# Kernel optimization log

Hardware: AMD Instinct MI355X
Metric: run time of the kernel (lower is better)

## Reference

```python
import jax, jax.numpy as jnp
import numpy as np

MAX_S, MIN_S, MAX_R = 3.0, 0.5, 3.0
A = (MAX_S - MIN_S) / 2.0   # 1.25
B = (MAX_S + MIN_S) / 2.0   # 1.75
C = (MAX_R - 1.0) / 2.0     # 1.0
D = (MAX_R + 1.0) / 2.0     # 2.0

# 3x3 kernel base points, row-major: dim0 = dy, dim1 = dx, shape [2, 9]
BASE = jnp.array([[-1, -1], [-1, 0], [-1, 1], [0, -1], [0, 0], [0, 1],
                  [1, -1], [1, 0], [1, 1]], dtype=jnp.float32).T


def conv2d(x, w, b=None):
    y = jax.lax.conv_general_dilated(x, w, window_strides=(1, 1),
                                     padding=((1, 1), (1, 1)),
                                     dimension_numbers=('NCHW', 'OIHW', 'NCHW'))
    if b is not None:
        y = y + b[None, :, None, None]
    return y


def setup_inputs() -> dict:
    key = jax.random.key(0)
    ks = jax.random.split(key, 8)
    return {
        'x': jax.random.normal(ks[0], (8, 64, 128, 128), jnp.float32),
        'w_main': jax.random.normal(ks[1], (64, 64, 3, 3), jnp.float32) * 0.05,
        'w_rot': jax.random.normal(ks[2], (2, 64, 3, 3), jnp.float32) * 0.05,
        'b_rot': jax.random.normal(ks[3], (2,), jnp.float32) * 0.05,
        'w_str': jax.random.normal(ks[4], (1, 64, 3, 3), jnp.float32) * 0.05,
        'b_str': jax.random.normal(ks[5], (1,), jnp.float32) * 0.05,
        'w_whl': jax.random.normal(ks[6], (1, 64, 3, 3), jnp.float32) * 0.05,
        'b_whl': jax.random.normal(ks[7], (1,), jnp.float32) * 0.05,
    }


def reference(x, w_main, w_rot, b_rot, w_str, b_str, w_whl, b_whl):
    b, c, H, W = x.shape
    K = 9
    # --- offset generation ---
    rot = conv2d(x, w_rot, b_rot)                     # [b,2,H,W]
    sin, cos = rot[:, 0], rot[:, 1]
    norm = jnp.sqrt(sin ** 2 + cos ** 2 + 1e-6)
    sin, cos = sin / norm, cos / norm
    r = jnp.tanh(conv2d(x, w_str, b_str))[:, 0] * A + B   # [b,H,W]
    wr = jnp.tanh(conv2d(x, w_whl, b_whl))[:, 0] * C + D  # [b,H,W]
    ky, kx = BASE[0], BASE[1]                             # [9]
    kyb = ky[None, :, None, None]
    kxb = kx[None, :, None, None]
    o0 = kyb * (wr * r)[:, None]                          # [b,9,H,W]
    o1 = kxb * wr[:, None]
    sinb, cosb = sin[:, None], cos[:, None]
    dy = cosb * o0 + sinb * o1 - kyb                      # rotation then subtract base
    dx = -sinb * o0 + cosb * o1 - kxb
    # --- deformable sampling positions (stride=1, pad=1, dil=1) ---
    py = jnp.arange(H, dtype=x.dtype)[None, None, :, None] + kyb + dy  # [b,9,H,W]
    px = jnp.arange(W, dtype=x.dtype)[None, None, None, :] + kxb + dx
    y0f = jnp.floor(py); x0f = jnp.floor(px)
    ly = py - y0f; lx = px - x0f
    y0 = y0f.astype(jnp.int32); x0 = x0f.astype(jnp.int32)
    x_flat = x.reshape(b, c, H * W)

    def gather(yi, xi, wgt):
        valid = (yi >= 0) & (yi < H) & (xi >= 0) & (xi < W)
        idx = jnp.clip(yi, 0, H - 1) * W + jnp.clip(xi, 0, W - 1)
        g = jnp.take_along_axis(x_flat, idx.reshape(b, 1, -1), axis=2)
        g = g.reshape(b, c, K, H, W)
        return g * (wgt * valid)[:, None]

    val = (gather(y0, x0, (1 - ly) * (1 - lx))
           + gather(y0, x0 + 1, (1 - ly) * lx)
           + gather(y0 + 1, x0, ly * (1 - lx))
           + gather(y0 + 1, x0 + 1, ly * lx))          # [b,c,9,H,W]
    # final 3x3 conv over sampled points == contraction over (c, k)
    out = jnp.einsum('bckhw,ock->bohw', val, w_main.reshape(w_main.shape[0], c, K))
    return out
```

## Files before the change

kernel.cpp:

```cpp
#include <hip/hip_runtime.h>
#include <hip/hip_bf16.h>
#include <hip/hip_fp16.h>
#include <math.h>

#define HH 128
#define WW 128
#define HWSZ (HH*WW)
#define CH 64
#define OC 64
#define NB 8
#define RG 28
#define RPX (RG*RG)

#define XT_BYTES   (16777216u)
#define OFFS_BYTES (2097152u)

typedef _Float16 f16x8 __attribute__((ext_vector_type(8)));
typedef __attribute__((ext_vector_type(4))) float f32x4_t;

__global__ __launch_bounds__(256) void transpose_kernel(
    const float* __restrict__ x, const float* __restrict__ w_main,
    __half* __restrict__ xT, __half* __restrict__ wmT2)
{
    const int t = threadIdx.x;
    const int i = blockIdx.x;
    if (i >= 2048) {
        const int base = (i - 2048) * 4096 + t * 16;
        #pragma unroll
        for (int j = 0; j < 16; ++j) {
            const int e = base + j;
            const int k = e >> 12;
            const int r = e & 4095;
            const int o = r >> 6;
            const int c = r & 63;
            wmT2[e] = __float2half(w_main[(size_t)o * (CH * 9) + c * 9 + k]);
        }
        return;
    }
    __shared__ float tile[64][65];
    const int b = i & 7;
    const int j = i >> 3;
    const int h  = j >> 1;
    const int w0 = (j & 1) * 64;
    const float* xb = x + (size_t)b * CH * HWSZ + h * WW + w0;
    {
        const int w = t & 63, c0 = (t >> 6) * 16;
        #pragma unroll
        for (int jj = 0; jj < 16; ++jj)
            tile[c0 + jj][w] = xb[(size_t)(c0 + jj) * HWSZ + w];
    }
    __syncthreads();
    {
        const int c = t & 63, wq = t >> 6;
        __half* o = xT + ((size_t)b * HWSZ + h * WW + w0) * 64;
        #pragma unroll
        for (int jj = 0; jj < 16; ++jj) {
            const int w = wq * 16 + jj;
            o[(size_t)w * 64 + c] = __float2half(tile[c][w]);
        }
    }
}

__global__ __launch_bounds__(256) void offsets_kernel(
    const float* __restrict__ x,
    const float* __restrict__ w_rot,
    const float* __restrict__ w_str,
    const float* __restrict__ w_whl,
    float4* __restrict__ part)
{
    __shared__ float xs[8][4][WW];
    const int t  = threadIdx.x;
    const int i  = blockIdx.x;
    const int b  = i & 7;
    const int rp = (i >> 3) & 63;
    const int cg = i >> 9;
    const int h0 = rp * 2;
    const int c0 = cg * 8;
    const float* xb = x + (size_t)b * CH * HWSZ;
    #pragma unroll
    for (int jj = 0; jj < 4; ++jj) {
        const int u   = t + jj * 256;
        const int ch  = u >> 7;
        const int rem = u & 127;
        const int row = rem >> 5;
        const int w4  = (rem & 31) * 4;
        const int grow = h0 - 1 + row;
        float4 v = make_float4(0.f, 0.f, 0.f, 0.f);
        if (grow >= 0 && grow < HH)
            v = *(const float4*)&xb[((size_t)(c0 + ch) * HH + grow) * WW + w4];
        *(float4*)&xs[ch][row][w4] = v;
    }
    __syncthreads();
    const int r = t >> 7, w = t & 127;
    const int wl = max(w - 1, 0), wr2 = min(w + 1, WW - 1);
    const float ml = (w > 0) ? 1.f : 0.f, mr = (w < WW - 1) ? 1.f : 0.f;
    float a0 = 0.f, a1 = 0.f, a2 = 0.f, a3 = 0.f;
    #pragma unroll
    for (int ch = 0; ch < 8; ++ch) {
        const int cc = c0 + ch;
        #pragma unroll
        for (int dy = 0; dy < 3; ++dy) {
            const float* row_ = &xs[ch][r + dy][0];
            const float nl = row_[wl] * ml;
            const float nc = row_[w];
            const float nr = row_[wr2] * mr;
            const int d0 = cc * 9 + dy * 3;
            a0 = fmaf(nl, w_rot[d0 + 0], a0); a0 = fmaf(nc, w_rot[d0 + 1], a0); a0 = fmaf(nr, w_rot[d0 + 2], a0);
            a1 = fmaf(nl, w_rot[576 + d0 + 0], a1); a1 = fmaf(nc, w_rot[576 + d0 + 1], a1); a1 = fmaf(nr, w_rot[576 + d0 + 2], a1);
            a2 = fmaf(nl, w_str[d0 + 0], a2); a2 = fmaf(nc, w_str[d0 + 1], a2); a2 = fmaf(nr, w_str[d0 + 2], a2);
            a3 = fmaf(nl, w_whl[d0 + 0], a3); a3 = fmaf(nc, w_whl[d0 + 1], a3); a3 = fmaf(nr, w_whl[d0 + 2], a3);
        }
    }
    part[((size_t)cg * NB + b) * HWSZ + (h0 + r) * WW + w] = make_float4(a0, a1, a2, a3);
}

__global__ __launch_bounds__(256) void reduce_kernel(
    const float4* __restrict__ part,
    const float* __restrict__ b_rot, const float* __restrict__ b_str,
    const float* __restrict__ b_whl, float4* __restrict__ offs)
{
    const int i = blockIdx.x * 256 + threadIdx.x;
    float4 s = make_float4(0.f, 0.f, 0.f, 0.f);
    #pragma unroll
    for (int cg = 0; cg < 8; ++cg) {
        const float4 p = part[(size_t)cg * NB * HWSZ + i];
        s.x += p.x; s.y += p.y; s.z += p.z; s.w += p.w;
    }
    float sv = s.x + b_rot[0], cv = s.y + b_rot[1];
    const float inv = 1.0f / sqrtf(sv * sv + cv * cv + 1e-6f);
    const float rr = tanhf(s.z + b_str[0]) * 1.25f + 1.75f;
    const float wq = tanhf(s.w + b_whl[0]) * 1.0f + 2.0f;
    offs[i] = make_float4(sv * inv, cv * inv, wq * rr, wq);
}

__global__ __launch_bounds__(256, 3) void deform_kernel(
    const __half* __restrict__ xT, const __half* __restrict__ wmT2,
    const float4* __restrict__ offs, float* __restrict__ out)
{
    __shared__ union {
        uint4 xs[RPX * 4];
        float ots[64][67];
    } sh;
    const int t  = threadIdx.x;
    const int wv = t >> 6;
    const int l  = t & 63;
    const int lm = l & 15;
    const int lg = l >> 4;
    const int i  = blockIdx.x;
    const int b  = i & 7;
    const int tile = i >> 3;
    const int w0 = (tile & 15) * 8;
    const int h0 = (tile >> 4) * 8;
    const int pi = wv * 16 + lm;
    const int h = h0 + (pi >> 3);
    const int w = w0 + (pi & 7);
    const float4 o4 = offs[(size_t)b * HWSZ + h * WW + w];
    const float sv = o4.x, cv = o4.y, av = o4.z, wvl = o4.w;
    const float hh  = (float)h;
    const float wwf = (float)w;
    const __half* xb = xT + (size_t)b * HWSZ * 64;

    int ti[9], td[9];
    __half2 w2[9][4];
    #pragma unroll
    for (int k = 0; k < 9; ++k) {
        const float kyf = (float)(k / 3) - 1.f;
        const float kxf = (float)(k % 3) - 1.f;
        const float o0v = kyf * av;
        const float o1v = kxf * wvl;
        const float pyf = hh  + cv * o0v + sv * o1v;
        const float pxf = wwf - sv * o0v + cv * o1v;
        const float y0f = floorf(pyf), x0f = floorf(pxf);
        const float ly = pyf - y0f, lx = pxf - x0f;
        const int y0 = (int)y0f, x0i = (int)x0f;
        const int y1 = y0 + 1, x1 = x0i + 1;
        const bool vy0 = (y0 >= 0) && (y0 < HH);
        const bool vy1 = (y1 >= 0) && (y1 < HH);
        const bool vx0 = (x0i >= 0) && (x0i < WW);
        const bool vx1 = (x1 >= 0) && (x1 < WW);
        w2[k][0] = __float2half2_rn((1.f - ly) * (1.f - lx) * ((vy0 && vx0) ? 1.f : 0.f));
        w2[k][1] = __float2half2_rn((1.f - ly) * lx         * ((vy0 && vx1) ? 1.f : 0.f));
        w2[k][2] = __float2half2_rn(ly * (1.f - lx)         * ((vy1 && vx0) ? 1.f : 0.f));
        w2[k][3] = __float2half2_rn(ly * lx                 * ((vy1 && vx1) ? 1.f : 0.f));
        const int iy0 = min(max(y0, 0), HH - 1), iy1 = min(max(y1, 0), HH - 1);
        const int ix0 = min(max(x0i, 0), WW - 1), ix1 = min(max(x1, 0), WW - 1);
        ti[k] = (iy0 - (h0 - 10)) * RG + (ix0 - (w0 - 10));
        td[k] = (ix1 - ix0) | ((iy1 - iy0) << 1);
    }

    f32x4_t acc0 = {0.f, 0.f, 0.f, 0.f};
    f32x4_t acc1 = acc0, acc2 = acc0, acc3 = acc0;

    for (int g = 0; g < 2; ++g) {
        __syncthreads();
        for (int u = t; u < RPX * 4; u += 256) {
            const int pxu = u >> 2, q = u & 3;
            const int lr = pxu / RG;
            const int lc = pxu - lr * RG;
            const int gy = min(max(h0 - 10 + lr, 0), HH - 1);
            const int gx = min(max(w0 - 10 + lc, 0), WW - 1);
            sh.xs[pxu * 4 + (q ^ (pxu & 3))] =
                *(const uint4*)(xb + (size_t)(gy * WW + gx) * 64 + g * 32 + q * 8);
        }
        __syncthreads();
        const int cb0 = g * 32 + lg * 8;
        #pragma unroll
        for (int k = 0; k < 9; ++k) {
            const int i00 = ti[k];
            const int dxx = td[k] & 1;
            const int dyy = (td[k] >> 1) * RG;
            const int i01 = i00 + dxx;
            const int i10 = i00 + dyy;
            const int i11 = i10 + dxx;
            union Q { uint4 q; __half2 h2[4]; };
            Q q00, q01, q10, q11;
            q00.q = sh.xs[i00 * 4 + (lg ^ (i00 & 3))];
            q01.q = sh.xs[i01 * 4 + (lg ^ (i01 & 3))];
            q10.q = sh.xs[i10 * 4 + (lg ^ (i10 & 3))];
            q11.q = sh.xs[i11 * 4 + (lg ^ (i11 & 3))];
            union { __half2 h2[4]; f16x8 v; } af;
            #pragma unroll
            for (int j = 0; j < 4; ++j) {
                af.h2[j] = __hfma2(q00.h2[j], w2[k][0],
                           __hfma2(q01.h2[j], w2[k][1],
                           __hfma2(q10.h2[j], w2[k][2],
                           __hmul2(q11.h2[j], w2[k][3]))));
            }
            const __half* wp = wmT2 + ((size_t)k * 64 + lm) * 64 + cb0;
            const f16x8 bf0 = *(const f16x8*)(wp);
            const f16x8 bf1 = *(const f16x8*)(wp + 1024);
            const f16x8 bf2v = *(const f16x8*)(wp + 2048);
            const f16x8 bf3 = *(const f16x8*)(wp + 3072);
            acc0 = __builtin_amdgcn_mfma_f32_16x16x32_f16(af.v, bf0,  acc0, 0, 0, 0);
            acc1 = __builtin_amdgcn_mfma_f32_16x16x32_f16(af.v, bf1,  acc1, 0, 0, 0);
            acc2 = __builtin_amdgcn_mfma_f32_16x16x32_f16(af.v, bf2v, acc2, 0, 0, 0);
            acc3 = __builtin_amdgcn_mfma_f32_16x16x32_f16(af.v, bf3,  acc3, 0, 0, 0);
        }
    }
    __syncthreads();
    const int pxw = wv * 16 + lg * 4;
    #pragma unroll
    for (int rg2 = 0; rg2 < 4; ++rg2) {
        sh.ots[pxw + rg2][ 0 + lm] = acc0[rg2];
        sh.ots[pxw + rg2][16 + lm] = acc1[rg2];
        sh.ots[pxw + rg2][32 + lm] = acc2[rg2];
        sh.ots[pxw + rg2][48 + lm] = acc3[rg2];
    }
    __syncthreads();
    const int oo = t >> 2;
    const int q  = (t & 3) * 16;
    #pragma unroll
    for (int j2 = 0; j2 < 4; ++j2) {
        const int px = q + j2 * 4;
        float4 v = make_float4(sh.ots[px + 0][oo], sh.ots[px + 1][oo],
                               sh.ots[px + 2][oo], sh.ots[px + 3][oo]);
        *(float4*)&out[((size_t)b * OC + oo) * HWSZ +
                       (h0 + (px >> 3)) * WW + w0 + (px & 7)] = v;
    }
}

extern "C" void kernel_launch(void* const* d_in, const int* in_sizes, int n_in,
                              void* d_out, int out_size, void* d_ws, size_t ws_size,
                              hipStream_t stream)
{
    const float* x      = (const float*)d_in[0];
    const float* w_main = (const float*)d_in[1];
    const float* w_rot  = (const float*)d_in[2];
    const float* b_rot  = (const float*)d_in[3];
    const float* w_str  = (const float*)d_in[4];
    const float* b_str  = (const float*)d_in[5];
    const float* w_whl  = (const float*)d_in[6];
    const float* b_whl  = (const float*)d_in[7];
    float* out = (float*)d_out;

    char* ws = (char*)d_ws;
    __half*  xT   = (__half*)ws;
    float4*  offs = (float4*)(ws + XT_BYTES);
    __half*  wmT2 = (__half*)(ws + XT_BYTES + OFFS_BYTES);
    float4*  part = (float4*)d_out;

    transpose_kernel<<<dim3(2057), 256, 0, stream>>>(x, w_main, xT, wmT2);
    offsets_kernel<<<dim3(4096), 256, 0, stream>>>(x, w_rot, w_str, w_whl, part);
    reduce_kernel<<<dim3(NB * HWSZ / 256), 256, 0, stream>>>(
        part, b_rot, b_str, b_whl, offs);
    deform_kernel<<<dim3(2048), 256, 0, stream>>>(xT, wmT2, offs, out);
}
```

Measured before the change: 213.1 us.

## Fuse transpose, offset conv and reduction into one pre-kernel; change LDS swizzle

Merges the transpose, offset-convolution and partial-sum reduction kernels into a single launch. Each offset block now loops over all 8 channel groups itself, so the partial-sum buffer and the separate reduce pass go away. This removes two launches and the partials round trip through global memory, but leaves only 512 offset blocks, each doing eight times more serial work. The deform kernel's LDS XOR swizzle now keys on (index>>1)&3 to change its bank-conflict pattern.

```diff
diff --git a/kernel.cpp b/kernel.cpp
--- a/kernel.cpp
+++ b/kernel.cpp
@@ -18,14 +18,21 @@
 typedef _Float16 f16x8 __attribute__((ext_vector_type(8)));
 typedef __attribute__((ext_vector_type(4))) float f32x4_t;
 
-__global__ __launch_bounds__(256) void transpose_kernel(
+__global__ __launch_bounds__(256) void pre_kernel(
     const float* __restrict__ x, const float* __restrict__ w_main,
-    __half* __restrict__ xT, __half* __restrict__ wmT2)
+    const float* __restrict__ w_rot, const float* __restrict__ w_str,
+    const float* __restrict__ w_whl,
+    const float* __restrict__ b_rot, const float* __restrict__ b_str,
+    const float* __restrict__ b_whl,
+    __half* __restrict__ xT, __half* __restrict__ wmT2,
+    float4* __restrict__ offs)
 {
+    __shared__ float shmem[64 * 65];
     const int t = threadIdx.x;
     const int i = blockIdx.x;
-    if (i >= 2048) {
-        const int base = (i - 2048) * 4096 + t * 16;
+
+    if (i >= 2560) {
+        const int base = (i - 2560) * 4096 + t * 16;
         #pragma unroll
         for (int j = 0; j < 16; ++j) {
             const int e = base + j;
@@ -37,100 +44,84 @@
         }
         return;
     }
-    __shared__ float tile[64][65];
-    const int b = i & 7;
-    const int j = i >> 3;
-    const int h  = j >> 1;
-    const int w0 = (j & 1) * 64;
-    const float* xb = x + (size_t)b * CH * HWSZ + h * WW + w0;
-    {
-        const int w = t & 63, c0 = (t >> 6) * 16;
-        #pragma unroll
-        for (int jj = 0; jj < 16; ++jj)
-            tile[c0 + jj][w] = xb[(size_t)(c0 + jj) * HWSZ + w];
-    }
-    __syncthreads();
-    {
-        const int c = t & 63, wq = t >> 6;
-        __half* o = xT + ((size_t)b * HWSZ + h * WW + w0) * 64;
-        #pragma unroll
-        for (int jj = 0; jj < 16; ++jj) {
-            const int w = wq * 16 + jj;
-            o[(size_t)w * 64 + c] = __float2half(tile[c][w]);
-        }
-    }
-}
-
-__global__ __launch_bounds__(256) void offsets_kernel(
-    const float* __restrict__ x,
-    const float* __restrict__ w_rot,
-    const float* __restrict__ w_str,
-    const float* __restrict__ w_whl,
-    float4* __restrict__ part)
-{
-    __shared__ float xs[8][4][WW];
-    const int t  = threadIdx.x;
-    const int i  = blockIdx.x;
+
+    if (i >= 512) {
+        float (*tile)[65] = (float(*)[65])shmem;
+        const int it = i - 512;
+        const int b = it & 7;
+        const int j = it >> 3;
+        const int h  = j >> 1;
+        const int w0 = (j & 1) * 64;
+        const float* xb = x + (size_t)b * CH * HWSZ + h * WW + w0;
+        {
+            const int w = t & 63, c0 = (t >> 6) * 16;
+            #pragma unroll
+            for (int jj = 0; jj < 16; ++jj)
+                tile[c0 + jj][w] = xb[(size_t)(c0 + jj) * HWSZ + w];
+        }
+        __syncthreads();
+        {
+            const int c = t & 63, wq = t >> 6;
+            __half* o = xT + ((size_t)b * HWSZ + h * WW + w0) * 64;
+            #pragma unroll
+            for (int jj = 0; jj < 16; ++jj) {
+                const int w = wq * 16 + jj;
+                o[(size_t)w * 64 + c] = __float2half(tile[c][w]);
+            }
+        }
+        return;
+    }
+
+    float (*xs)[4][WW] = (float(*)[4][WW])shmem;
     const int b  = i & 7;
-    const int rp = (i >> 3) & 63;
-    const int cg = i >> 9;
+    const int rp = i >> 3;
     const int h0 = rp * 2;
-    const int c0 = cg * 8;
     const float* xb = x + (size_t)b * CH * HWSZ;
-    #pragma unroll
-    for (int jj = 0; jj < 4; ++jj) {
-        const int u   = t + jj * 256;
-        const int ch  = u >> 7;
-        const int rem = u & 127;
-        const int row = rem >> 5;
-        const int w4  = (rem & 31) * 4;
-        const int grow = h0 - 1 + row;
-        float4 v = make_float4(0.f, 0.f, 0.f, 0.f);
-        if (grow >= 0 && grow < HH)
-            v = *(const float4*)&xb[((size_t)(c0 + ch) * HH + grow) * WW + w4];
-        *(float4*)&xs[ch][row][w4] = v;
-    }
-    __syncthreads();
     const int r = t >> 7, w = t & 127;
     const int wl = max(w - 1, 0), wr2 = min(w + 1, WW - 1);
     const float ml = (w > 0) ? 1.f : 0.f, mr = (w < WW - 1) ? 1.f : 0.f;
     float a0 = 0.f, a1 = 0.f, a2 = 0.f, a3 = 0.f;
-    #pragma unroll
-    for (int ch = 0; ch < 8; ++ch) {
-        const int cc = c0 + ch;
-        #pragma unroll
-        for (int dy = 0; dy < 3; ++dy) {
-            const float* row_ = &xs[ch][r + dy][0];
-            const float nl = row_[wl] * ml;
-            const float nc = row_[w];
-            const float nr = row_[wr2] * mr;
-            const int d0 = cc * 9 + dy * 3;
-            a0 = fmaf(nl, w_rot[d0 + 0], a0); a0 = fmaf(nc, w_rot[d0 + 1], a0); a0 = fmaf(nr, w_rot[d0 + 2], a0);
-            a1 = fmaf(nl, w_rot[576 + d0 + 0], a1); a1 = fmaf(nc, w_rot[576 + d0 + 1], a1); a1 = fmaf(nr, w_rot[576 + d0 + 2], a1);
-            a2 = fmaf(nl, w_str[d0 + 0], a2); a2 = fmaf(nc, w_str[d0 + 1], a2); a2 = fmaf(nr, w_str[d0 + 2], a2);
-            a3 = fmaf(nl, w_whl[d0 + 0], a3); a3 = fmaf(nc, w_whl[d0 + 1], a3); a3 = fmaf(nr, w_whl[d0 + 2], a3);
-        }
-    }
-    part[((size_t)cg * NB + b) * HWSZ + (h0 + r) * WW + w] = make_float4(a0, a1, a2, a3);
-}
-
-__global__ __launch_bounds__(256) void reduce_kernel(
-    const float4* __restrict__ part,
-    const float* __restrict__ b_rot, const float* __restrict__ b_str,
-    const float* __restrict__ b_whl, float4* __restrict__ offs)
-{
-    const int i = blockIdx.x * 256 + threadIdx.x;
-    float4 s = make_float4(0.f, 0.f, 0.f, 0.f);
-    #pragma unroll
+
     for (int cg = 0; cg < 8; ++cg) {
-        const float4 p = part[(size_t)cg * NB * HWSZ + i];
-        s.x += p.x; s.y += p.y; s.z += p.z; s.w += p.w;
-    }
-    float sv = s.x + b_rot[0], cv = s.y + b_rot[1];
+        const int c0 = cg * 8;
+        __syncthreads();
+        #pragma unroll
+        for (int jj = 0; jj < 4; ++jj) {
+            const int u   = t + jj * 256;
+            const int ch  = u >> 7;
+            const int rem = u & 127;
+            const int row = rem >> 5;
+            const int w4  = (rem & 31) * 4;
+            const int grow = h0 - 1 + row;
+            float4 v = make_float4(0.f, 0.f, 0.f, 0.f);
+            if (grow >= 0 && grow < HH)
+                v = *(const float4*)&xb[((size_t)(c0 + ch) * HH + grow) * WW + w4];
+            *(float4*)&xs[ch][row][w4] = v;
+        }
+        __syncthreads();
+        #pragma unroll
+        for (int ch = 0; ch < 8; ++ch) {
+            const int cc = c0 + ch;
+            #pragma unroll
+            for (int dy = 0; dy < 3; ++dy) {
+                const float* row_ = &xs[ch][r + dy][0];
+                const float nl = row_[wl] * ml;
+                const float nc = row_[w];
+                const float nr = row_[wr2] * mr;
+                const int d0 = cc * 9 + dy * 3;
+                a0 = fmaf(nl, w_rot[d0 + 0], a0); a0 = fmaf(nc, w_rot[d0 + 1], a0); a0 = fmaf(nr, w_rot[d0 + 2], a0);
+                a1 = fmaf(nl, w_rot[576 + d0 + 0], a1); a1 = fmaf(nc, w_rot[576 + d0 + 1], a1); a1 = fmaf(nr, w_rot[576 + d0 + 2], a1);
+                a2 = fmaf(nl, w_str[d0 + 0], a2); a2 = fmaf(nc, w_str[d0 + 1], a2); a2 = fmaf(nr, w_str[d0 + 2], a2);
+                a3 = fmaf(nl, w_whl[d0 + 0], a3); a3 = fmaf(nc, w_whl[d0 + 1], a3); a3 = fmaf(nr, w_whl[d0 + 2], a3);
+            }
+        }
+    }
+
+    float sv = a0 + b_rot[0], cv = a1 + b_rot[1];
     const float inv = 1.0f / sqrtf(sv * sv + cv * cv + 1e-6f);
-    const float rr = tanhf(s.z + b_str[0]) * 1.25f + 1.75f;
-    const float wq = tanhf(s.w + b_whl[0]) * 1.0f + 2.0f;
-    offs[i] = make_float4(sv * inv, cv * inv, wq * rr, wq);
+    const float rr = tanhf(a2 + b_str[0]) * 1.25f + 1.75f;
+    const float wq = tanhf(a3 + b_whl[0]) * 1.0f + 2.0f;
+    offs[(size_t)b * HWSZ + (h0 + r) * WW + w] = make_float4(sv * inv, cv * inv, wq * rr, wq);
 }
 
 __global__ __launch_bounds__(256, 3) void deform_kernel(
@@ -199,7 +190,7 @@
             const int lc = pxu - lr * RG;
             const int gy = min(max(h0 - 10 + lr, 0), HH - 1);
             const int gx = min(max(w0 - 10 + lc, 0), WW - 1);
-            sh.xs[pxu * 4 + (q ^ (pxu & 3))] =
+            sh.xs[pxu * 4 + (q ^ ((pxu >> 1) & 3))] =
                 *(const uint4*)(xb + (size_t)(gy * WW + gx) * 64 + g * 32 + q * 8);
         }
         __syncthreads();
@@ -214,10 +205,10 @@
             const int i11 = i10 + dxx;
             union Q { uint4 q; __half2 h2[4]; };
             Q q00, q01, q10, q11;
-            q00.q = sh.xs[i00 * 4 + (lg ^ (i00 & 3))];
-            q01.q = sh.xs[i01 * 4 + (lg ^ (i01 & 3))];
-            q10.q = sh.xs[i10 * 4 + (lg ^ (i10 & 3))];
-            q11.q = sh.xs[i11 * 4 + (lg ^ (i11 & 3))];
+            q00.q = sh.xs[i00 * 4 + (lg ^ ((i00 >> 1) & 3))];
+            q01.q = sh.xs[i01 * 4 + (lg ^ ((i01 >> 1) & 3))];
+            q10.q = sh.xs[i10 * 4 + (lg ^ ((i10 >> 1) & 3))];
+            q11.q = sh.xs[i11 * 4 + (lg ^ ((i11 >> 1) & 3))];
             union { __half2 h2[4]; f16x8 v; } af;
             #pragma unroll
             for (int j = 0; j < 4; ++j) {
@@ -237,6 +228,7 @@
             acc3 = __builtin_amdgcn_mfma_f32_16x16x32_f16(af.v, bf3,  acc3, 0, 0, 0);
         }
     }
+
     __syncthreads();
     const int pxw = wv * 16 + lg * 4;
     #pragma unroll
@@ -277,11 +269,9 @@
     __half*  xT   = (__half*)ws;
     float4*  offs = (float4*)(ws + XT_BYTES);
     __half*  wmT2 = (__half*)(ws + XT_BYTES + OFFS_BYTES);
-    float4*  part = (float4*)d_out;
-
-    transpose_kernel<<<dim3(2057), 256, 0, stream>>>(x, w_main, xT, wmT2);
-    offsets_kernel<<<dim3(4096), 256, 0, stream>>>(x, w_rot, w_str, w_whl, part);
-    reduce_kernel<<<dim3(NB * HWSZ / 256), 256, 0, stream>>>(
-        part, b_rot, b_str, b_whl, offs);
+
+    pre_kernel<<<dim3(2569), 256, 0, stream>>>(x, w_main, w_rot, w_str, w_whl,
+                                               b_rot, b_str, b_whl,
+                                               xT, wmT2, offs);
     deform_kernel<<<dim3(2048), 256, 0, stream>>>(xT, wmT2, offs, out);
 }
```

Measured after the change: 215.0 us. No clear change (+0.9%).
